# Optimization experiments

Hardware: AMD Instinct MI355X
Metric: run time of the kernel (lower is better)

Reference implementation:

```python
import jax, jax.numpy as jnp
import numpy as np

L_V, L_T, D, H, HID = 1024, 128, 4096, 8, 2048
N1 = L_V // 2      # tokens kept by selector module 1
N2 = N1 // 2       # tokens kept by selector module 2 (final selected)
N_REM = L_V - N2   # remaining tokens to merge


def setup_inputs() -> dict:
    key = jax.random.key(0)
    ks = jax.random.split(key, 8)
    s = 0.02
    return {
        "vision_feature": jax.random.normal(ks[0], (L_V, D), jnp.float32),
        "text_embed": jax.random.normal(ks[1], (L_T, D), jnp.float32),
        "attention_mask": jnp.ones((L_T,), jnp.int32),
        # stacked MHA params, order: [m1.global, m1.local, m2.global, m2.local]
        "attn_in_w": s * jax.random.normal(ks[2], (4, 3 * D, D), jnp.float32),
        "attn_in_b": jnp.zeros((4, 3 * D), jnp.float32),
        "attn_out_w": s * jax.random.normal(ks[3], (4, D, D), jnp.float32),
        "attn_out_b": jnp.zeros((4, D), jnp.float32),
        # stacked MLP params, order: [module1, module2]
        "mlp_w1": s * jax.random.normal(ks[4], (2, HID, D), jnp.float32),
        "mlp_b1": jnp.zeros((2, HID), jnp.float32),
        "mlp_w2": s * jax.random.normal(ks[5], (2, HID), jnp.float32),
        "mlp_b2": jnp.zeros((2,), jnp.float32),
    }


def _mha(xq, xkv, in_w, in_b, out_w, out_b):
    # torch nn.MultiheadAttention (unbatched, eval mode: no dropout)
    dh = D // H
    qw, kw, vw = jnp.split(in_w, 3, axis=0)
    qb, kb, vb = jnp.split(in_b, 3)
    q = (xq @ qw.T + qb).reshape(-1, H, dh)
    k = (xkv @ kw.T + kb).reshape(-1, H, dh)
    v = (xkv @ vw.T + vb).reshape(-1, H, dh)
    scores = jnp.einsum('qhd,khd->hqk', q, k) * (1.0 / np.sqrt(dh))
    attn = jax.nn.softmax(scores, axis=-1)
    o = jnp.einsum('hqk,khd->qhd', attn, v).reshape(-1, D)
    return o @ out_w.T + out_b


def _select(vf, te, pg, pl, w1, b1, w2, b2, n_keep):
    # TokenSelectionModule (deterministic top-k selection path, fixed shapes)
    comb = jnp.concatenate([vf, te], axis=0)
    g = _mha(vf, comb, *pg)
    l = _mha(vf, te, *pl) + vf
    x = jnp.stack([l, g], axis=1)                      # (L, 2, D): 0=local, 1=global
    h = jax.nn.relu(jnp.einsum('lcd,hd->lch', x, w1) + b1)
    logits = jnp.einsum('lch,h->lc', h, w2) + b2       # (L, 2)
    _, idx = jax.lax.top_k(logits[:, 1], n_keep)
    return vf[idx], idx


def _forward(vision_feature, text_embed, attn_in_w, attn_in_b, attn_out_w,
             attn_out_b, mlp_w1, mlp_b1, mlp_w2, mlp_b2):
    p = lambda i: (attn_in_w[i], attn_in_b[i], attn_out_w[i], attn_out_b[i])
    sv1, idx1 = _select(vision_feature, text_embed, p(0), p(1),
                        mlp_w1[0], mlp_b1[0], mlp_w2[0], mlp_b2[0], N1)
    sel, idx2 = _select(sv1, text_embed, p(2), p(3),
                        mlp_w1[1], mlp_b1[1], mlp_w2[1], mlp_b2[1], N2)
    sel_idx = idx1[idx2]

    # remaining = complement of selected indices (fixed size N_REM)
    sel_mask = jnp.zeros((L_V,), bool).at[sel_idx].set(True)
    rem_idx = jnp.nonzero(~sel_mask, size=N_REM)[0]
    rem = vision_feature[rem_idx]                      # (N_REM, D)

    # cosine similarity (torch eps=1e-8) + argmax matching
    nr = jnp.linalg.norm(rem, axis=-1)
    ns = jnp.linalg.norm(sel, axis=-1)
    sim = (rem @ sel.T) / jnp.maximum(nr[:, None] * ns[None, :], 1e-8)
    best = jnp.argmax(sim, axis=1)                     # (N_REM,) cluster ids

    # per-cluster gather+mean+normalize merge, vectorized as segment reduces
    cnt = jax.ops.segment_sum(jnp.ones((N_REM,), jnp.float32), best, num_segments=N2)
    sum_rem = jax.ops.segment_sum(rem, best, num_segments=N2)
    mean = (sel + sum_rem) / (cnt + 1.0)[:, None]
    seg_max = jax.ops.segment_max(nr, best, num_segments=N2)
    max_norm = jnp.maximum(ns, jnp.where(cnt > 0, seg_max, 0.0))
    mean_unit = mean / jnp.linalg.norm(mean, axis=-1, keepdims=True)
    updated = jnp.where((cnt > 0)[:, None], mean_unit * max_norm[:, None], sel)
    return updated  # top_k == 0 path: return merged selected features


def reference(vision_feature, text_embed, attention_mask, attn_in_w, attn_in_b,
              attn_out_w, attn_out_b, mlp_w1, mlp_b1, mlp_w2, mlp_b2):
    # attention_mask is accepted but unused, matching the torch forward
    return _forward(vision_feature, text_embed, attn_in_w, attn_in_b,
                    attn_out_w, attn_out_b, mlp_w1, mlp_b1, mlp_w2, mlp_b2)
```

## Files before the change

### kernel.cpp

```cpp
#include <hip/hip_runtime.h>
#include <hip/hip_bf16.h>
#include <math.h>
#include <stdint.h>

typedef __attribute__((ext_vector_type(4))) float f32x4;
typedef __attribute__((ext_vector_type(8))) short s16x8;
typedef __attribute__((ext_vector_type(4))) short s16x4;

struct sh2 { short hi, lo; };

__device__ __forceinline__ sh2 splitf(float x)
{
    __hip_bfloat16 h = __float2bfloat16(x);
    float hf = __bfloat162float(h);
    __hip_bfloat16 l = __float2bfloat16(x - hf);
    sh2 r;
    r.hi = __builtin_bit_cast(short, h);
    r.lo = __builtin_bit_cast(short, l);
    return r;
}

__device__ __forceinline__ void split8(const float4& a, const float4& b,
                                       s16x8& h, s16x8& l)
{
    sh2 p;
    p = splitf(a.x); h[0] = p.hi; l[0] = p.lo;
    p = splitf(a.y); h[1] = p.hi; l[1] = p.lo;
    p = splitf(a.z); h[2] = p.hi; l[2] = p.lo;
    p = splitf(a.w); h[3] = p.hi; l[3] = p.lo;
    p = splitf(b.x); h[4] = p.hi; l[4] = p.lo;
    p = splitf(b.y); h[5] = p.hi; l[5] = p.lo;
    p = splitf(b.z); h[6] = p.hi; l[6] = p.lo;
    p = splitf(b.w); h[7] = p.hi; l[7] = p.lo;
}

typedef const __attribute__((address_space(1))) void gvoid_t;
typedef __attribute__((address_space(3))) void lvoid_t;
__device__ __forceinline__ void gld_lds16(const void* g, void* l)
{
    __builtin_amdgcn_global_load_lds((gvoid_t*)(uintptr_t)g,
                                     (lvoid_t*)(uintptr_t)l, 16, 0, 0);
}

template<int BF, int EPI, bool RELU>
__global__ __launch_bounds__(256, 2) void mfma_gemm(
    const short* __restrict__ Ahi, const short* __restrict__ Alo, int lda, long sA,
    const float* __restrict__ Bf, const short* __restrict__ Bhi,
    const short* __restrict__ Blo, int ldb, long sB,
    float* __restrict__ Cf, short* __restrict__ Chi, short* __restrict__ Clo,
    short* __restrict__ Thi, short* __restrict__ Tlo, int ldc, int ldT, long sC,
    int K, int SK, float alpha, const float* __restrict__ bias)
{
    __shared__ short SH[2][16384];
    const int zf = blockIdx.z;
    const int sk = (SK > 1) ? (zf % SK) : 0;
    const int bz = (SK > 1) ? (zf / SK) : zf;
    const int Kc = K / SK;
    const int kb = sk * Kc;
    Ahi += (long)bz * sA; Alo += (long)bz * sA;
    if (BF == 0) Bf += (long)bz * sB; else { Bhi += (long)bz * sB; Blo += (long)bz * sB; }
    const long cofs = (long)((SK > 1) ? zf : bz) * sC;

    const int GX = gridDim.x, GY = gridDim.y;
    const int nwg = GX * GY;
    const int bid = blockIdx.x + GX * blockIdx.y;
    const int q8 = nwg >> 3, r8 = nwg & 7;
    const int xcd = bid & 7, sl = bid >> 3;
    const int t = (xcd < r8) ? (xcd * (q8 + 1) + sl)
                             : (r8 * (q8 + 1) + (xcd - r8) * q8 + sl);
    const int m0 = (t % GY) * 128, n0 = (t / GY) * 128;

    const int tid = threadIdx.x;
    const int lane = tid & 63, wave = tid >> 6;
    const int wr = (wave >> 1) * 64, wc = (wave & 1) * 64;
    const int lrow = lane & 15, lk = lane >> 4;
    const int cswz8 = (lk ^ ((lrow >> 1) & 3)) << 3;

    const int rA0 = wave * 16 + (lane >> 2);
    const int rA1 = rA0 + 64;
    const int sc0 = ((lane & 3) ^ ((rA0 >> 1) & 3)) * 8;
    const int sc1 = ((lane & 3) ^ ((rA1 >> 1) & 3)) * 8;
    const long gA0 = (long)(m0 + rA0) * lda + sc0;
    const long gA1 = (long)(m0 + rA1) * lda + sc1;
    long gB0 = 0, gB1 = 0;
    if (BF == 1) {
        gB0 = (long)(n0 + rA0) * ldb + sc0;
        gB1 = (long)(n0 + rA1) * ldb + sc1;
    }
    const int lw0 = wave * 512, lw1 = wave * 512 + 2048;

    const int brow = tid & 127;
    const int bkc0 = (tid >> 7) * 8;
    const int bkc1 = bkc0 + 16;
    const int bw0 = brow * 32 + (((bkc0 >> 3) ^ ((brow >> 1) & 3)) << 3);
    const int bw1 = brow * 32 + (((bkc1 >> 3) ^ ((brow >> 1) & 3)) << 3);
    const float* bpr = (BF == 0) ? Bf + (long)(n0 + brow) * ldb : nullptr;

    f32x4 acc[4][4];
#pragma unroll
    for (int i = 0; i < 4; i++)
#pragma unroll
        for (int j = 0; j < 4; j++) acc[i][j] = (f32x4){0.f, 0.f, 0.f, 0.f};

    float4 rb0a, rb0b, rb1a, rb1b;

    {
        short* S = &SH[0][0];
        gld_lds16(Ahi + gA0 + kb, S + lw0);
        gld_lds16(Ahi + gA1 + kb, S + lw1);
        gld_lds16(Alo + gA0 + kb, S + 4096 + lw0);
        gld_lds16(Alo + gA1 + kb, S + 4096 + lw1);
        if constexpr (BF == 1) {
            gld_lds16(Bhi + gB0 + kb, S + 8192 + lw0);
            gld_lds16(Bhi + gB1 + kb, S + 8192 + lw1);
            gld_lds16(Blo + gB0 + kb, S + 12288 + lw0);
            gld_lds16(Blo + gB1 + kb, S + 12288 + lw1);
        } else {
            rb0a = *(const float4*)(bpr + kb + bkc0);
            rb0b = *(const float4*)(bpr + kb + bkc0 + 4);
            rb1a = *(const float4*)(bpr + kb + bkc1);
            rb1b = *(const float4*)(bpr + kb + bkc1 + 4);
            s16x8 h, l;
            split8(rb0a, rb0b, h, l);
            *(s16x8*)&S[8192 + bw0] = h;
            *(s16x8*)&S[12288 + bw0] = l;
            split8(rb1a, rb1b, h, l);
            *(s16x8*)&S[8192 + bw1] = h;
            *(s16x8*)&S[12288 + bw1] = l;
        }
    }
    __syncthreads();

    int cur = 0;
    const int kend = kb + Kc;
    for (int k0 = kb; k0 < kend; k0 += 32) {
        const int kn = k0 + 32;
        const bool nx = (kn < kend);
        short* SN = &SH[cur ^ 1][0];
        if (nx) {
            gld_lds16(Ahi + gA0 + kn, SN + lw0);
            gld_lds16(Ahi + gA1 + kn, SN + lw1);
            gld_lds16(Alo + gA0 + kn, SN + 4096 + lw0);
            gld_lds16(Alo + gA1 + kn, SN + 4096 + lw1);
            if constexpr (BF == 1) {
                gld_lds16(Bhi + gB0 + kn, SN + 8192 + lw0);
                gld_lds16(Bhi + gB1 + kn, SN + 8192 + lw1);
                gld_lds16(Blo + gB0 + kn, SN + 12288 + lw0);
                gld_lds16(Blo + gB1 + kn, SN + 12288 + lw1);
            } else {
                rb0a = *(const float4*)(bpr + kn + bkc0);
                rb0b = *(const float4*)(bpr + kn + bkc0 + 4);
                rb1a = *(const float4*)(bpr + kn + bkc1);
                rb1b = *(const float4*)(bpr + kn + bkc1 + 4);
            }
        }
        const short* S = &SH[cur][0];
        s16x8 ah[4], al[4];
#pragma unroll
        for (int m = 0; m < 4; m++) {
            const int idx = (wr + m * 16 + lrow) * 32 + cswz8;
            ah[m] = *(const s16x8*)&S[idx];
            al[m] = *(const s16x8*)&S[4096 + idx];
        }
#pragma unroll
        for (int n = 0; n < 4; n++) {
            const int idx = (wc + n * 16 + lrow) * 32 + cswz8;
            const s16x8 bh = *(const s16x8*)&S[8192 + idx];
            const s16x8 bl = *(const s16x8*)&S[12288 + idx];
#pragma unroll
            for (int m = 0; m < 4; m++) {
                acc[m][n] = __builtin_amdgcn_mfma_f32_16x16x32_bf16(ah[m], bh, acc[m][n], 0, 0, 0);
                acc[m][n] = __builtin_amdgcn_mfma_f32_16x16x32_bf16(ah[m], bl, acc[m][n], 0, 0, 0);
                acc[m][n] = __builtin_amdgcn_mfma_f32_16x16x32_bf16(al[m], bh, acc[m][n], 0, 0, 0);
            }
        }
        if (BF == 0 && nx) {
            s16x8 h, l;
            split8(rb0a, rb0b, h, l);
            *(s16x8*)&SN[8192 + bw0] = h;
            *(s16x8*)&SN[12288 + bw0] = l;
            split8(rb1a, rb1b, h, l);
            *(s16x8*)&SN[8192 + bw1] = h;
            *(s16x8*)&SN[12288 + bw1] = l;
        }
        __syncthreads();
        cur ^= 1;
    }
#pragma unroll
    for (int n = 0; n < 4; n++) {
        const int col = n0 + wc + n * 16 + lrow;
        const float bv = (SK == 1 && bias) ? bias[col] : 0.f;
#pragma unroll
        for (int m = 0; m < 4; m++) {
            const int row = m0 + wr + m * 16 + lk * 4;
            if (SK > 1) {
#pragma unroll
                for (int r = 0; r < 4; r++)
                    Cf[cofs + (long)(row + r) * ldc + col] = acc[m][n][r] * alpha;
            } else if constexpr (EPI == 0) {
#pragma unroll
                for (int r = 0; r < 4; r++) {
                    float v = acc[m][n][r] * alpha + bv;
                    if (RELU) v = fmaxf(v, 0.f);
                    Cf[cofs + (long)(row + r) * ldc + col] = v;
                }
            } else if constexpr (EPI == 1) {
#pragma unroll
                for (int r = 0; r < 4; r++) {
                    float v = acc[m][n][r] * alpha + bv;
                    sh2 p = splitf(v);
                    Chi[cofs + (long)(row + r) * ldc + col] = p.hi;
                    Clo[cofs + (long)(row + r) * ldc + col] = p.lo;
                }
            } else {
                if (n0 < 8192) {
#pragma unroll
                    for (int r = 0; r < 4; r++) {
                        float v = acc[m][n][r] + bv;
                        sh2 p = splitf(v);
                        Chi[(long)(row + r) * ldc + col] = p.hi;
                        Clo[(long)(row + r) * ldc + col] = p.lo;
                    }
                } else {
                    s16x4 h4, l4;
#pragma unroll
                    for (int r = 0; r < 4; r++) {
                        float v = acc[m][n][r] + bv;
                        sh2 p = splitf(v);
                        h4[r] = p.hi; l4[r] = p.lo;
                    }
                    const long tof = (long)(col - 8192) * ldT + row;
                    *(s16x4*)&Thi[tof] = h4;
                    *(s16x4*)&Tlo[tof] = l4;
                }
            }
        }
    }
}

__global__ __launch_bounds__(512, 2) void mfma_gemm256(
    const short* __restrict__ Ahi, const short* __restrict__ Alo, int lda,
    const float* __restrict__ Bf, int ldb,
    short* __restrict__ Chi, short* __restrict__ Clo,
    short* __restrict__ Thi, short* __restrict__ Tlo, int ldc, int ldT,
    int K, int Mreal, const float* __restrict__ bias)
{
    __shared__ short SH[2][32768];

    const int GX = gridDim.x, GY = gridDim.y;
    const int nwg = GX * GY;
    const int bid = blockIdx.x + GX * blockIdx.y;
    const int q8 = nwg >> 3, r8 = nwg & 7;
    const int xcd = bid & 7, sl = bid >> 3;
    const int t = (xcd < r8) ? (xcd * (q8 + 1) + sl)
                             : (r8 * (q8 + 1) + (xcd - r8) * q8 + sl);
    const int m0 = (t % GY) * 256, n0 = (t / GY) * 256;

    const int tid = threadIdx.x;
    const int lane = tid & 63, wave = tid >> 6;
    const int wr = (wave >> 1) * 64, wc = (wave & 1) * 128;
    const int lrow = lane & 15, lk = lane >> 4;
    const int cswz8 = (lk ^ ((lrow >> 1) & 3)) << 3;

    const int rA0 = wave * 32 + (lane >> 2);
    const int rA1 = rA0 + 16;
    const int sc0 = ((lane & 3) ^ ((rA0 >> 1) & 3)) * 8;
    const int sc1 = ((lane & 3) ^ ((rA1 >> 1) & 3)) * 8;
    const long gA0 = (long)(m0 + rA0) * lda + sc0;
    const long gA1 = (long)(m0 + rA1) * lda + sc1;
    const int lw0 = wave * 1024, lw1 = wave * 1024 + 512;

    const int brow = tid & 255;
    const int bk = (tid >> 8) * 16;
    const int bw0 = brow * 32 + ((((bk >> 3) + 0) ^ ((brow >> 1) & 3)) << 3);
    const int bw1 = brow * 32 + ((((bk >> 3) + 1) ^ ((brow >> 1) & 3)) << 3);
    const float* bpr = Bf + (long)(n0 + brow) * ldb + bk;

    f32x4 acc[4][8];
#pragma unroll
    for (int i = 0; i < 4; i++)
#pragma unroll
        for (int j = 0; j < 8; j++) acc[i][j] = (f32x4){0.f, 0.f, 0.f, 0.f};

    float4 rb0, rb1, rb2, rb3;

    {
        short* S = &SH[0][0];
        gld_lds16(Ahi + gA0, S + lw0);
        gld_lds16(Ahi + gA1, S + lw1);
        gld_lds16(Alo + gA0, S + 8192 + lw0);
        gld_lds16(Alo + gA1, S + 8192 + lw1);
        rb0 = *(const float4*)(bpr + 0);
        rb1 = *(const float4*)(bpr + 4);
        rb2 = *(const float4*)(bpr + 8);
        rb3 = *(const float4*)(bpr + 12);
        s16x8 h, l;
        split8(rb0, rb1, h, l);
        *(s16x8*)&S[16384 + bw0] = h;
        *(s16x8*)&S[24576 + bw0] = l;
        split8(rb2, rb3, h, l);
        *(s16x8*)&S[16384 + bw1] = h;
        *(s16x8*)&S[24576 + bw1] = l;
    }
    __syncthreads();

    int cur = 0;
    for (int k0 = 0; k0 < K; k0 += 32) {
        const int kn = k0 + 32;
        const bool nx = (kn < K);
        short* SN = &SH[cur ^ 1][0];
        if (nx) {
            gld_lds16(Ahi + gA0 + kn, SN + lw0);
            gld_lds16(Ahi + gA1 + kn, SN + lw1);
            gld_lds16(Alo + gA0 + kn, SN + 8192 + lw0);
            gld_lds16(Alo + gA1 + kn, SN + 8192 + lw1);
            rb0 = *(const float4*)(bpr + kn + 0);
            rb1 = *(const float4*)(bpr + kn + 4);
            rb2 = *(const float4*)(bpr + kn + 8);
            rb3 = *(const float4*)(bpr + kn + 12);
        }
        const short* S = &SH[cur][0];
        s16x8 ah[4], al[4];
#pragma unroll
        for (int m = 0; m < 4; m++) {
            const int idx = (wr + m * 16 + lrow) * 32 + cswz8;
            ah[m] = *(const s16x8*)&S[idx];
            al[m] = *(const s16x8*)&S[8192 + idx];
        }
#pragma unroll
        for (int n = 0; n < 8; n++) {
            const int idx = (wc + n * 16 + lrow) * 32 + cswz8;
            const s16x8 bh = *(const s16x8*)&S[16384 + idx];
            const s16x8 bl = *(const s16x8*)&S[24576 + idx];
#pragma unroll
            for (int m = 0; m < 4; m++) {
                acc[m][n] = __builtin_amdgcn_mfma_f32_16x16x32_bf16(ah[m], bh, acc[m][n], 0, 0, 0);
                acc[m][n] = __builtin_amdgcn_mfma_f32_16x16x32_bf16(ah[m], bl, acc[m][n], 0, 0, 0);
                acc[m][n] = __builtin_amdgcn_mfma_f32_16x16x32_bf16(al[m], bh, acc[m][n], 0, 0, 0);
            }
        }
        if (nx) {
            s16x8 h, l;
            split8(rb0, rb1, h, l);
            *(s16x8*)&SN[16384 + bw0] = h;
            *(s16x8*)&SN[24576 + bw0] = l;
            split8(rb2, rb3, h, l);
            *(s16x8*)&SN[16384 + bw1] = h;
            *(s16x8*)&SN[24576 + bw1] = l;
        }
        __syncthreads();
        cur ^= 1;
    }
#pragma unroll
    for (int n = 0; n < 8; n++) {
        const int col = n0 + wc + n * 16 + lrow;
        const float bv = bias[col];
#pragma unroll
        for (int m = 0; m < 4; m++) {
            const int row = m0 + wr + m * 16 + lk * 4;
            if (row < Mreal) {
                if (n0 < 8192) {
#pragma unroll
                    for (int r = 0; r < 4; r++) {
                        float v = acc[m][n][r] + bv;
                        sh2 p = splitf(v);
                        Chi[(long)(row + r) * ldc + col] = p.hi;
                        Clo[(long)(row + r) * ldc + col] = p.lo;
                    }
                } else {
                    s16x4 h4, l4;
#pragma unroll
                    for (int r = 0; r < 4; r++) {
                        float v = acc[m][n][r] + bv;
                        sh2 p = splitf(v);
                        h4[r] = p.hi; l4[r] = p.lo;
                    }
                    const long tof = (long)(col - 8192) * ldT + row;
                    *(s16x4*)&Thi[tof] = h4;
                    *(s16x4*)&Tlo[tof] = l4;
                }
            }
        }
    }
}

template<int EPI, bool RELU>
__global__ __launch_bounds__(256) void reduce_k(
    const float* __restrict__ P, long zstride, int SK, int total,
    int Ninner, int ldc, int colstep,
    float* __restrict__ Cf, short* __restrict__ Chi, short* __restrict__ Clo,
    const float* __restrict__ bias)
{
    const int bz = blockIdx.y;
    const long pbase = (long)bz * SK * zstride;
    const int e = (blockIdx.x * 256 + threadIdx.x) * 4;
    if (e >= total) return;
    const float* p = P + pbase + e;
    float4 s = *(const float4*)p;
    for (int k = 1; k < SK; k++) {
        float4 tv = *(const float4*)(p + (long)k * zstride);
        s.x += tv.x; s.y += tv.y; s.z += tv.z; s.w += tv.w;
    }
    const int r = e / Ninner, c = e % Ninner;
    const int col0 = colstep * bz + c;
    const long ob = (long)r * ldc + col0;
    float v[4] = {s.x, s.y, s.z, s.w};
#pragma unroll
    for (int j = 0; j < 4; j++) {
        float x = v[j] + (bias ? bias[col0 + j] : 0.f);
        if (RELU) x = fmaxf(x, 0.f);
        if constexpr (EPI == 0) {
            Cf[ob + j] = x;
        } else {
            sh2 pp = splitf(x);
            Chi[ob + j] = pp.hi;
            Clo[ob + j] = pp.lo;
        }
    }
}

__global__ __launch_bounds__(256) void split_rows(
    const float* __restrict__ src, const int* __restrict__ map,
    short* __restrict__ dhi, short* __restrict__ dlo)
{
    const int r = blockIdx.x;
    const int sr = map ? map[r] : r;
    const float4* s = (const float4*)(src + (long)sr * 4096);
    const long db = (long)r * 4096;
    for (int i = threadIdx.x; i < 1024; i += 256) {
        float4 f = s[i];
        s16x4 h, l;
        sh2 p;
        p = splitf(f.x); h[0] = p.hi; l[0] = p.lo;
        p = splitf(f.y); h[1] = p.hi; l[1] = p.lo;
        p = splitf(f.z); h[2] = p.hi; l[2] = p.lo;
        p = splitf(f.w); h[3] = p.hi; l[3] = p.lo;
        *(s16x4*)&dhi[db + i * 4] = h;
        *(s16x4*)&dlo[db + i * 4] = l;
    }
}

__global__ __launch_bounds__(256) void softmax_split(
    const float* __restrict__ x, short* __restrict__ phi, short* __restrict__ plo,
    int cols)
{
    const long rb = (long)blockIdx.x * cols;
    const float4* xr = (const float4*)(x + rb);
    const int t = threadIdx.x;
    const int n4 = cols >> 2;
    __shared__ float red[256];
    float mx = -INFINITY;
    for (int i = t; i < n4; i += 256) {
        float4 f = xr[i];
        mx = fmaxf(fmaxf(mx, fmaxf(f.x, f.y)), fmaxf(f.z, f.w));
    }
    red[t] = mx; __syncthreads();
    for (int off = 128; off; off >>= 1) { if (t < off) red[t] = fmaxf(red[t], red[t + off]); __syncthreads(); }
    mx = red[0]; __syncthreads();
    float4 ebuf[2];
    float s = 0.f;
    int nb = 0;
    for (int i = t; i < n4; i += 256) {
        float4 f = xr[i];
        f.x = expf(f.x - mx); f.y = expf(f.y - mx); f.z = expf(f.z - mx); f.w = expf(f.w - mx);
        ebuf[nb++] = f;
        s += f.x + f.y + f.z + f.w;
    }
    red[t] = s; __syncthreads();
    for (int off = 128; off; off >>= 1) { if (t < off) red[t] += red[t + off]; __syncthreads(); }
    s = red[0];
    nb = 0;
    for (int i = t; i < n4; i += 256) {
        float4 f = ebuf[nb++];
        f.x /= s; f.y /= s; f.z /= s; f.w /= s;
        s16x4 h, l;
        sh2 p;
        p = splitf(f.x); h[0] = p.hi; l[0] = p.lo;
        p = splitf(f.y); h[1] = p.hi; l[1] = p.lo;
        p = splitf(f.z); h[2] = p.hi; l[2] = p.lo;
        p = splitf(f.w); h[3] = p.hi; l[3] = p.lo;
        *(s16x4*)&phi[rb + i * 4] = h;
        *(s16x4*)&plo[rb + i * 4] = l;
    }
}

__global__ __launch_bounds__(256) void gemv_kernel(
    const float* __restrict__ H, const float* __restrict__ w2,
    const float* __restrict__ b2, float* __restrict__ logits)
{
    const int r = blockIdx.x, t = threadIdx.x;
    const float* row = H + (long)r * 2048;
    float s = 0.f;
    for (int c = t; c < 2048; c += 256) s += row[c] * w2[c];
    __shared__ float red[256];
    red[t] = s; __syncthreads();
    for (int off = 128; off; off >>= 1) { if (t < off) red[t] += red[t + off]; __syncthreads(); }
    if (!t) logits[r] = red[0] + b2[0];
}

__global__ void topk_kernel(const float* __restrict__ vals, int n, int k, int* __restrict__ out)
{
    __shared__ float sv[1024];
    __shared__ int   si[1024];
    const int t = threadIdx.x;
    sv[t] = vals[t]; si[t] = t;
    for (int size = 2; size <= n; size <<= 1) {
        for (int stride = size >> 1; stride > 0; stride >>= 1) {
            __syncthreads();
            const int j = t ^ stride;
            if (j > t) {
                float av = sv[t], bv = sv[j];
                int ai = si[t], bi = si[j];
                const bool before = (av > bv) || (av == bv && ai < bi);
                const bool dir = ((t & size) == 0);
                if (dir ? !before : before) { sv[t] = bv; si[t] = bi; sv[j] = av; si[j] = ai; }
            }
        }
    }
    __syncthreads();
    if (t < k) out[t] = si[t];
}

__global__ void gather_sel_kernel(const int* __restrict__ idx1, const int* __restrict__ idx2,
                                  int* __restrict__ selidx)
{
    const int t = threadIdx.x;
    if (t < 256) selidx[t] = idx1[idx2[t]];
}

__global__ void complement_kernel(const int* __restrict__ selidx, int* __restrict__ remidx)
{
    __shared__ int mask[1024];
    __shared__ int scan[1024];
    const int t = threadIdx.x;
    mask[t] = 0;
    __syncthreads();
    if (t < 256) mask[selidx[t]] = 1;
    __syncthreads();
    const int keep = 1 - mask[t];
    scan[t] = keep;
    __syncthreads();
    for (int off = 1; off < 1024; off <<= 1) {
        int v = scan[t];
        if (t >= off) v += scan[t - off];
        __syncthreads();
        scan[t] = v;
        __syncthreads();
    }
    if (keep) remidx[scan[t] - 1] = t;
}

__global__ __launch_bounds__(256) void gather_rows_kernel(
    float* __restrict__ dst, const float* __restrict__ src,
    const int* __restrict__ map, int ncols)
{
    const int r = blockIdx.x;
    const int sr = map[r];
    const float4* s = (const float4*)(src + (long)sr * ncols);
    float4* d = (float4*)(dst + (long)r * ncols);
    for (int i = threadIdx.x; i < ncols / 4; i += 256) d[i] = s[i];
}

__global__ __launch_bounds__(256) void rownorm_kernel(
    const float* __restrict__ x, float* __restrict__ out)
{
    const int r = blockIdx.x, t = threadIdx.x;
    const float* row = x + (long)r * 4096;
    float s = 0.f;
    for (int c = t; c < 4096; c += 256) { float v = row[c]; s += v * v; }
    __shared__ float red[256];
    red[t] = s; __syncthreads();
    for (int off = 128; off; off >>= 1) { if (t < off) red[t] += red[t + off]; __syncthreads(); }
    if (!t) out[r] = sqrtf(red[0]);
}

__global__ __launch_bounds__(256) void argmax_kernel(
    const float* __restrict__ S, const float* __restrict__ nr,
    const float* __restrict__ ns, int* __restrict__ best)
{
    const int r = blockIdx.x, t = threadIdx.x;
    float v = S[(long)r * 256 + t] / fmaxf(nr[r] * ns[t], 1e-8f);
    __shared__ float bv[256];
    __shared__ int bi[256];
    bv[t] = v; bi[t] = t; __syncthreads();
    for (int off = 128; off; off >>= 1) {
        if (t < off) {
            float ov = bv[t + off]; int oi = bi[t + off];
            if (ov > bv[t] || (ov == bv[t] && oi < bi[t])) { bv[t] = ov; bi[t] = oi; }
        }
        __syncthreads();
    }
    if (!t) best[r] = bi[0];
}

__global__ __launch_bounds__(256) void merge_kernel(
    const float* __restrict__ selb, const float* __restrict__ rem,
    const int* __restrict__ best, const float* __restrict__ nr,
    const float* __restrict__ ns, float* __restrict__ out)
{
    const int j = blockIdx.x, t = threadIdx.x;
    __shared__ int sbest[768];
    __shared__ float snr[768];
    __shared__ float red[256];
    for (int i = t; i < 768; i += 256) { sbest[i] = best[i]; snr[i] = nr[i]; }
    __syncthreads();
    float acc[16];
#pragma unroll
    for (int d = 0; d < 16; d++) acc[d] = 0.f;
    int cnt = 0; float smax = 0.f;
    const int base = t * 16;
    for (int i = 0; i < 768; i++) {
        if (sbest[i] == j) {
            cnt++;
            smax = fmaxf(smax, snr[i]);
            const float* rp = rem + (long)i * 4096 + base;
#pragma unroll
            for (int d = 0; d < 16; d += 4) {
                float4 x4 = *(const float4*)(rp + d);
                acc[d] += x4.x; acc[d + 1] += x4.y; acc[d + 2] += x4.z; acc[d + 3] += x4.w;
            }
        }
    }
    const float* sp = selb + (long)j * 4096 + base;
    float mean[16]; float ss = 0.f;
    const float denom = (float)(cnt + 1);
#pragma unroll
    for (int d = 0; d < 16; d++) { mean[d] = (sp[d] + acc[d]) / denom; ss += mean[d] * mean[d]; }
    red[t] = ss; __syncthreads();
    for (int off = 128; off; off >>= 1) { if (t < off) red[t] += red[t + off]; __syncthreads(); }
    const float nm = sqrtf(red[0]);
    const float mx = fmaxf(ns[j], cnt > 0 ? smax : 0.f);
    float* op = out + (long)j * 4096 + base;
#pragma unroll
    for (int d = 0; d < 16; d++) op[d] = (cnt > 0) ? (mean[d] / nm) * mx : sp[d];
}

extern "C" void kernel_launch(void* const* d_in, const int* in_sizes, int n_in,
                              void* d_out, int out_size, void* d_ws, size_t ws_size,
                              hipStream_t stream)
{
    const float* vf   = (const float*)d_in[0];
    const float* te   = (const float*)d_in[1];
    const float* inw  = (const float*)d_in[3];
    const float* inb  = (const float*)d_in[4];
    const float* outw = (const float*)d_in[5];
    const float* outb = (const float*)d_in[6];
    const float* w1   = (const float*)d_in[7];
    const float* b1   = (const float*)d_in[8];
    const float* w2   = (const float*)d_in[9];
    const float* b2   = (const float*)d_in[10];
    float* out = (float*)d_out;
    char* base = (char*)d_ws;

    char* qkR = base;
    char* vTR = base + 37748736;
    char* scR = vTR + 18874368;
    float* smalls = (float*)(scR + 37748736);

    short* qkhi = (short*)qkR;
    short* qklo = (short*)(qkR + 18874368);
    short* vThi = (short*)vTR;
    short* vTlo = (short*)(vTR + 9437184);
    float* hbuf = (float*)scR;

    float* logits = smalls;
    float* nr     = smalls + 1024;
    float* ns     = smalls + 1792;
    int* idx1   = (int*)(smalls + 2048);
    int* idx2   = (int*)(smalls + 2560);
    int* selidx = (int*)(smalls + 2816);
    int* remidx = (int*)(smalls + 3072);
    int* best   = (int*)(smalls + 3840);

    const float scl = (float)(1.0 / sqrt(512.0));

    for (int m = 0; m < 2; m++) {
        const int Mq  = m ? 512 : 1024;
        const int Mkv = m ? 640 : 1152;
        const float* Wqkv = inw + (size_t)(2 * m) * 12288 * 4096;
        const float* bqkv = inb + (size_t)(2 * m) * 12288;
        const float* ow = outw + (size_t)(2 * m) * 4096 * 4096;
        const float* ob = outb + (size_t)(2 * m) * 4096;

        short* chi = (short*)scR;
        short* clo = (short*)(scR + (size_t)Mkv * 4096 * 2);
        if (m == 0) {
            split_rows<<<1024, 256, 0, stream>>>(vf, nullptr, chi, clo);
            split_rows<<<128, 256, 0, stream>>>(te, nullptr,
                chi + (size_t)1024 * 4096, clo + (size_t)1024 * 4096);
        } else {
            split_rows<<<512, 256, 0, stream>>>(vf, idx1, chi, clo);
            split_rows<<<128, 256, 0, stream>>>(te, nullptr,
                chi + (size_t)512 * 4096, clo + (size_t)512 * 4096);
        }
        if (m == 0) {
            mfma_gemm256<<<dim3(48, 5, 1), 512, 0, stream>>>(
                chi, clo, 4096, Wqkv, 4096, qkhi, qklo, vThi, vTlo,
                8192, 1152, 4096, 1152, bqkv);
        } else {
            mfma_gemm<0, 2, false><<<dim3(96, Mkv / 128, 1), 256, 0, stream>>>(
                chi, clo, 4096, 0, Wqkv, nullptr, nullptr, 4096, 0,
                nullptr, qkhi, qklo, vThi, vTlo, 8192, 1152, 0, 4096, 1, 1.f, bqkv);
        }
        float* scor = (float*)(m ? (scR + 10485760) : scR);
        mfma_gemm<1, 0, false><<<dim3(Mkv / 128, Mq / 128, 8), 256, 0, stream>>>(
            qkhi, qklo, 8192, 512, nullptr, qkhi + 4096, qklo + 4096, 8192, 512,
            scor, nullptr, nullptr, nullptr, nullptr, Mkv, 0, (long)Mq * Mkv,
            512, 1, scl, nullptr);
        short* phi = (short*)qkR;
        short* plo = (short*)(qkR + (size_t)8 * Mq * Mkv * 2);
        softmax_split<<<8 * Mq, 256, 0, stream>>>(scor, phi, plo, Mkv);
        short* ohi = (short*)scR;
        short* olo = (short*)(scR + (size_t)Mq * 4096 * 2);
        if (m == 0) {
            mfma_gemm<1, 1, false><<<dim3(4, 8, 8), 256, 0, stream>>>(
                phi, plo, Mkv, (long)Mq * Mkv, nullptr, vThi, vTlo, 1152, 512L * 1152,
                nullptr, ohi, olo, nullptr, nullptr, 4096, 0, 512, Mkv, 1, 1.f, nullptr);
        } else {
            float* Ppv = (float*)(qkR + 20971520);
            mfma_gemm<1, 0, false><<<dim3(4, 4, 16), 256, 0, stream>>>(
                phi, plo, Mkv, (long)Mq * Mkv, nullptr, vThi, vTlo, 1152, 512L * 1152,
                Ppv, nullptr, nullptr, nullptr, nullptr, 512, 0, 262144,
                Mkv, 2, 1.f, nullptr);
            reduce_k<1, false><<<dim3(256, 8), 256, 0, stream>>>(
                Ppv, 262144, 2, 262144, 512, 4096, 512, nullptr, ohi, olo, nullptr);
        }
        short* ghi = (short*)(scR + (size_t)Mq * 4096 * 4);
        short* glo = (short*)(scR + (size_t)Mq * 4096 * 6);
        {
            float* Pg = (float*)qkR;
            const long zst = (long)Mq * 4096;
            mfma_gemm<0, 0, false><<<dim3(32, Mq / 128, 2), 256, 0, stream>>>(
                ohi, olo, 4096, 0, ow, nullptr, nullptr, 4096, 0,
                Pg, nullptr, nullptr, nullptr, nullptr, 4096, 0, zst,
                4096, 2, 1.f, nullptr);
            reduce_k<1, false><<<dim3((int)(zst / 1024), 1), 256, 0, stream>>>(
                Pg, zst, 2, (int)zst, 4096, 4096, 0, nullptr, ghi, glo, ob);
        }
        {
            float* Pm = (float*)(qkR + 8388608);
            const long zst = (long)Mq * 2048;
            mfma_gemm<0, 0, false><<<dim3(16, Mq / 128, 4), 256, 0, stream>>>(
                ghi, glo, 4096, 0, w1 + (size_t)m * 2048 * 4096, nullptr, nullptr, 4096, 0,
                Pm, nullptr, nullptr, nullptr, nullptr, 2048, 0, zst,
                4096, 4, 1.f, nullptr);
            reduce_k<0, true><<<dim3((int)(zst / 1024), 1), 256, 0, stream>>>(
                Pm, zst, 4, (int)zst, 2048, 2048, 0, hbuf, nullptr, nullptr,
                b1 + (size_t)m * 2048);
        }
        gemv_kernel<<<Mq, 256, 0, stream>>>(hbuf, w2 + (size_t)m * 2048, b2 + m, logits);
        if (m == 0) topk_kernel<<<1, 1024, 0, stream>>>(logits, 1024, 512, idx1);
        else        topk_kernel<<<1, 512, 0, stream>>>(logits, 512, 256, idx2);
    }

    short* remhi = (short*)scR;
    short* remlo = (short*)(scR + 6291456);
    short* selhi = (short*)(scR + 12582912);
    short* sello = (short*)(scR + 14680064);
    float* rem_f = (float*)(scR + 16777216);
    float* sel_f = (float*)(scR + 29360128);
    float* Smat  = (float*)(scR + 33554432);

    gather_sel_kernel<<<1, 256, 0, stream>>>(idx1, idx2, selidx);
    complement_kernel<<<1, 1024, 0, stream>>>(selidx, remidx);
    split_rows<<<768, 256, 0, stream>>>(vf, remidx, remhi, remlo);
    split_rows<<<256, 256, 0, stream>>>(vf, selidx, selhi, sello);
    gather_rows_kernel<<<768, 256, 0, stream>>>(rem_f, vf, remidx, 4096);
    gather_rows_kernel<<<256, 256, 0, stream>>>(sel_f, vf, selidx, 4096);
    rownorm_kernel<<<768, 256, 0, stream>>>(rem_f, nr);
    rownorm_kernel<<<256, 256, 0, stream>>>(sel_f, ns);
    {
        float* Ps = (float*)qkR;
        mfma_gemm<1, 0, false><<<dim3(2, 6, 8), 256, 0, stream>>>(
            remhi, remlo, 4096, 0, nullptr, selhi, sello, 4096, 0,
            Ps, nullptr, nullptr, nullptr, nullptr, 256, 0, 196608,
            4096, 8, 1.f, nullptr);
        reduce_k<0, false><<<dim3(192, 1), 256, 0, stream>>>(
            Ps, 196608, 8, 196608, 256, 256, 0, Smat, nullptr, nullptr, nullptr);
    }
    argmax_kernel<<<768, 256, 0, stream>>>(Smat, nr, ns, best);
    merge_kernel<<<256, 256, 0, stream>>>(sel_f, rem_f, best, nr, ns, out);
}
```

Before: 1.301 ms.

## Reorder MFMA issue in GEMM inner loops and fuse small prep kernels

Both MFMA GEMM kernels now load all B fragments first and issue the three split-bf16 MFMA passes as separate sweeps, so consecutive MFMAs target different accumulators instead of chaining on one. The vf/text split launches are merged into one split_comb kernel, and the gather, complement, split, copy and row-norm kernels before the merge step are fused into sel_complement_kernel and prep_merge. The goal is fewer MFMA dependency stalls and less launch and memory-pass overhead, at the cost of more live registers in the GEMM loops.

```diff
diff --git a/kernel.cpp b/kernel.cpp
--- a/kernel.cpp
+++ b/kernel.cpp
@@ -155,7 +155,7 @@
             }
         }
         const short* S = &SH[cur][0];
-        s16x8 ah[4], al[4];
+        s16x8 ah[4], al[4], bh[4], bl[4];
 #pragma unroll
         for (int m = 0; m < 4; m++) {
             const int idx = (wr + m * 16 + lrow) * 32 + cswz8;
@@ -165,15 +165,24 @@
 #pragma unroll
         for (int n = 0; n < 4; n++) {
             const int idx = (wc + n * 16 + lrow) * 32 + cswz8;
-            const s16x8 bh = *(const s16x8*)&S[8192 + idx];
-            const s16x8 bl = *(const s16x8*)&S[12288 + idx];
-#pragma unroll
-            for (int m = 0; m < 4; m++) {
-                acc[m][n] = __builtin_amdgcn_mfma_f32_16x16x32_bf16(ah[m], bh, acc[m][n], 0, 0, 0);
-                acc[m][n] = __builtin_amdgcn_mfma_f32_16x16x32_bf16(ah[m], bl, acc[m][n], 0, 0, 0);
-                acc[m][n] = __builtin_amdgcn_mfma_f32_16x16x32_bf16(al[m], bh, acc[m][n], 0, 0, 0);
-            }
-        }
+            bh[n] = *(const s16x8*)&S[8192 + idx];
+            bl[n] = *(const s16x8*)&S[12288 + idx];
+        }
+#pragma unroll
+        for (int n = 0; n < 4; n++)
+#pragma unroll
+            for (int m = 0; m < 4; m++)
+                acc[m][n] = __builtin_amdgcn_mfma_f32_16x16x32_bf16(ah[m], bh[n], acc[m][n], 0, 0, 0);
+#pragma unroll
+        for (int n = 0; n < 4; n++)
+#pragma unroll
+            for (int m = 0; m < 4; m++)
+                acc[m][n] = __builtin_amdgcn_mfma_f32_16x16x32_bf16(ah[m], bl[n], acc[m][n], 0, 0, 0);
+#pragma unroll
+        for (int n = 0; n < 4; n++)
+#pragma unroll
+            for (int m = 0; m < 4; m++)
+                acc[m][n] = __builtin_amdgcn_mfma_f32_16x16x32_bf16(al[m], bh[n], acc[m][n], 0, 0, 0);
         if (BF == 0 && nx) {
             s16x8 h, l;
             split8(rb0a, rb0b, h, l);
@@ -328,16 +337,29 @@
             al[m] = *(const s16x8*)&S[8192 + idx];
         }
 #pragma unroll
-        for (int n = 0; n < 8; n++) {
-            const int idx = (wc + n * 16 + lrow) * 32 + cswz8;
-            const s16x8 bh = *(const s16x8*)&S[16384 + idx];
-            const s16x8 bl = *(const s16x8*)&S[24576 + idx];
-#pragma unroll
-            for (int m = 0; m < 4; m++) {
-                acc[m][n] = __builtin_amdgcn_mfma_f32_16x16x32_bf16(ah[m], bh, acc[m][n], 0, 0, 0);
-                acc[m][n] = __builtin_amdgcn_mfma_f32_16x16x32_bf16(ah[m], bl, acc[m][n], 0, 0, 0);
-                acc[m][n] = __builtin_amdgcn_mfma_f32_16x16x32_bf16(al[m], bh, acc[m][n], 0, 0, 0);
+        for (int np = 0; np < 4; np++) {
+            s16x8 bh[2], bl[2];
+#pragma unroll
+            for (int j = 0; j < 2; j++) {
+                const int idx = (wc + (np * 2 + j) * 16 + lrow) * 32 + cswz8;
+                bh[j] = *(const s16x8*)&S[16384 + idx];
+                bl[j] = *(const s16x8*)&S[24576 + idx];
             }
+#pragma unroll
+            for (int j = 0; j < 2; j++)
+#pragma unroll
+                for (int m = 0; m < 4; m++)
+                    acc[m][np * 2 + j] = __builtin_amdgcn_mfma_f32_16x16x32_bf16(ah[m], bh[j], acc[m][np * 2 + j], 0, 0, 0);
+#pragma unroll
+            for (int j = 0; j < 2; j++)
+#pragma unroll
+                for (int m = 0; m < 4; m++)
+                    acc[m][np * 2 + j] = __builtin_amdgcn_mfma_f32_16x16x32_bf16(ah[m], bl[j], acc[m][np * 2 + j], 0, 0, 0);
+#pragma unroll
+            for (int j = 0; j < 2; j++)
+#pragma unroll
+                for (int m = 0; m < 4; m++)
+                    acc[m][np * 2 + j] = __builtin_amdgcn_mfma_f32_16x16x32_bf16(al[m], bh[j], acc[m][np * 2 + j], 0, 0, 0);
         }
         if (nx) {
             s16x8 h, l;
@@ -419,13 +441,16 @@
     }
 }
 
-__global__ __launch_bounds__(256) void split_rows(
-    const float* __restrict__ src, const int* __restrict__ map,
+__global__ __launch_bounds__(256) void split_comb(
+    const float* __restrict__ vf, const float* __restrict__ te,
+    const int* __restrict__ map, int Mvf,
     short* __restrict__ dhi, short* __restrict__ dlo)
 {
     const int r = blockIdx.x;
-    const int sr = map ? map[r] : r;
-    const float4* s = (const float4*)(src + (long)sr * 4096);
+    const float* srow;
+    if (r < Mvf) srow = vf + (long)(map ? map[r] : r) * 4096;
+    else         srow = te + (long)(r - Mvf) * 4096;
+    const float4* s = (const float4*)srow;
     const long db = (long)r * 4096;
     for (int i = threadIdx.x; i < 1024; i += 256) {
         float4 f = s[i];
@@ -521,21 +546,21 @@
     if (t < k) out[t] = si[t];
 }
 
-__global__ void gather_sel_kernel(const int* __restrict__ idx1, const int* __restrict__ idx2,
-                                  int* __restrict__ selidx)
-{
-    const int t = threadIdx.x;
-    if (t < 256) selidx[t] = idx1[idx2[t]];
-}
-
-__global__ void complement_kernel(const int* __restrict__ selidx, int* __restrict__ remidx)
+__global__ void sel_complement_kernel(const int* __restrict__ idx1,
+                                      const int* __restrict__ idx2,
+                                      int* __restrict__ selidx,
+                                      int* __restrict__ remidx)
 {
     __shared__ int mask[1024];
     __shared__ int scan[1024];
     const int t = threadIdx.x;
     mask[t] = 0;
     __syncthreads();
-    if (t < 256) mask[selidx[t]] = 1;
+    if (t < 256) {
+        const int s = idx1[idx2[t]];
+        selidx[t] = s;
+        mask[s] = 1;
+    }
     __syncthreads();
     const int keep = 1 - mask[t];
     scan[t] = keep;
@@ -550,28 +575,41 @@
     if (keep) remidx[scan[t] - 1] = t;
 }
 
-__global__ __launch_bounds__(256) void gather_rows_kernel(
-    float* __restrict__ dst, const float* __restrict__ src,
-    const int* __restrict__ map, int ncols)
-{
-    const int r = blockIdx.x;
-    const int sr = map[r];
-    const float4* s = (const float4*)(src + (long)sr * ncols);
-    float4* d = (float4*)(dst + (long)r * ncols);
-    for (int i = threadIdx.x; i < ncols / 4; i += 256) d[i] = s[i];
-}
-
-__global__ __launch_bounds__(256) void rownorm_kernel(
-    const float* __restrict__ x, float* __restrict__ out)
-{
-    const int r = blockIdx.x, t = threadIdx.x;
-    const float* row = x + (long)r * 4096;
-    float s = 0.f;
-    for (int c = t; c < 4096; c += 256) { float v = row[c]; s += v * v; }
+__global__ __launch_bounds__(256) void prep_merge(
+    const float* __restrict__ vf,
+    const int* __restrict__ remidx, const int* __restrict__ selidx,
+    float* __restrict__ rem_f, float* __restrict__ sel_f,
+    short* __restrict__ remhi, short* __restrict__ remlo,
+    short* __restrict__ selhi, short* __restrict__ sello,
+    float* __restrict__ nr, float* __restrict__ ns)
+{
+    const int b = blockIdx.x, t = threadIdx.x;
+    const bool isrem = (b < 768);
+    const int r = isrem ? b : b - 768;
+    const int sr = isrem ? remidx[r] : selidx[r];
+    const float4* s = (const float4*)(vf + (long)sr * 4096);
+    float* dstF = (isrem ? rem_f : sel_f) + (long)r * 4096;
+    short* dhi = (isrem ? remhi : selhi) + (long)r * 4096;
+    short* dlo = (isrem ? remlo : sello) + (long)r * 4096;
+    for (int i = t; i < 1024; i += 256) {
+        float4 f = s[i];
+        *(float4*)&dstF[i * 4] = f;
+        s16x4 h, l;
+        sh2 p;
+        p = splitf(f.x); h[0] = p.hi; l[0] = p.lo;
+        p = splitf(f.y); h[1] = p.hi; l[1] = p.lo;
+        p = splitf(f.z); h[2] = p.hi; l[2] = p.lo;
+        p = splitf(f.w); h[3] = p.hi; l[3] = p.lo;
+        *(s16x4*)&dhi[i * 4] = h;
+        *(s16x4*)&dlo[i * 4] = l;
+    }
+    __syncthreads();
+    float ss = 0.f;
+    for (int c = t; c < 4096; c += 256) { float v = dstF[c]; ss += v * v; }
     __shared__ float red[256];
-    red[t] = s; __syncthreads();
+    red[t] = ss; __syncthreads();
     for (int off = 128; off; off >>= 1) { if (t < off) red[t] += red[t + off]; __syncthreads(); }
-    if (!t) out[r] = sqrtf(red[0]);
+    if (!t) (isrem ? nr : ns)[r] = sqrtf(red[0]);
 }
 
 __global__ __launch_bounds__(256) void argmax_kernel(
@@ -684,15 +722,7 @@
 
         short* chi = (short*)scR;
         short* clo = (short*)(scR + (size_t)Mkv * 4096 * 2);
-        if (m == 0) {
-            split_rows<<<1024, 256, 0, stream>>>(vf, nullptr, chi, clo);
-            split_rows<<<128, 256, 0, stream>>>(te, nullptr,
-                chi + (size_t)1024 * 4096, clo + (size_t)1024 * 4096);
-        } else {
-            split_rows<<<512, 256, 0, stream>>>(vf, idx1, chi, clo);
-            split_rows<<<128, 256, 0, stream>>>(te, nullptr,
-                chi + (size_t)512 * 4096, clo + (size_t)512 * 4096);
-        }
+        split_comb<<<Mkv, 256, 0, stream>>>(vf, te, m ? idx1 : nullptr, Mq, chi, clo);
         if (m == 0) {
             mfma_gemm256<<<dim3(48, 5, 1), 512, 0, stream>>>(
                 chi, clo, 4096, Wqkv, 4096, qkhi, qklo, vThi, vTlo,
@@ -761,14 +791,9 @@
     float* sel_f = (float*)(scR + 29360128);
     float* Smat  = (float*)(scR + 33554432);
 
-    gather_sel_kernel<<<1, 256, 0, stream>>>(idx1, idx2, selidx);
-    complement_kernel<<<1, 1024, 0, stream>>>(selidx, remidx);
-    split_rows<<<768, 256, 0, stream>>>(vf, remidx, remhi, remlo);
-    split_rows<<<256, 256, 0, stream>>>(vf, selidx, selhi, sello);
-    gather_rows_kernel<<<768, 256, 0, stream>>>(rem_f, vf, remidx, 4096);
-    gather_rows_kernel<<<256, 256, 0, stream>>>(sel_f, vf, selidx, 4096);
-    rownorm_kernel<<<768, 256, 0, stream>>>(rem_f, nr);
-    rownorm_kernel<<<256, 256, 0, stream>>>(sel_f, ns);
+    sel_complement_kernel<<<1, 1024, 0, stream>>>(idx1, idx2, selidx, remidx);
+    prep_merge<<<1024, 256, 0, stream>>>(vf, remidx, selidx, rem_f, sel_f,
+                                         remhi, remlo, selhi, sello, nr, ns);
     {
         float* Ps = (float*)qkR;
         mfma_gemm<1, 0, false><<<dim3(2, 6, 8), 256, 0, stream>>>(
```

Result: no change. 1.307 ms (+0.5%).
